# Kernel tuning notes

Hardware: AMD Instinct MI355X
Metric: run time of the kernel (lower is better)

Reference implementation:

```python
import jax, jax.numpy as jnp
import numpy as np

D_MODEL = 512
H = 8
D_K = D_MODEL // H


def setup_inputs() -> dict:
    key = jax.random.key(0)
    ks = jax.random.split(key, 11)
    B, S = 2, 2048
    scale = 1.0 / np.sqrt(D_MODEL)
    return {
        "q": jax.random.normal(ks[0], (B, S, D_MODEL), jnp.float32),
        "v": jax.random.normal(ks[1], (B, S, D_MODEL), jnp.float32),
        "k": jax.random.normal(ks[2], (B, S, D_MODEL), jnp.float32),
        "w_q": jax.random.normal(ks[3], (D_MODEL, D_MODEL), jnp.float32) * scale,
        "b_q": jnp.zeros((D_MODEL,), jnp.float32),
        "w_k": jax.random.normal(ks[4], (D_MODEL, D_MODEL), jnp.float32) * scale,
        "b_k": jnp.zeros((D_MODEL,), jnp.float32),
        "w_v": jax.random.normal(ks[5], (D_MODEL, D_MODEL), jnp.float32) * scale,
        "b_v": jnp.zeros((D_MODEL,), jnp.float32),
        "w_o": jax.random.normal(ks[6], (D_MODEL, D_MODEL), jnp.float32) * scale,
        "b_o": jnp.zeros((D_MODEL,), jnp.float32),
    }


def reference(q, v, k, w_q, b_q, w_k, b_k, w_v, b_v, w_o, b_o):
    B, S, _ = q.shape
    # projections (nn.Linear: x @ W.T + b)
    query = q @ w_q.T + b_q
    key_t = k @ w_k.T + b_k
    value = v @ w_v.T + b_v
    # split heads: [B, S, H, D_K] -> [B, H, S, D_K]
    query = query.reshape(B, S, H, D_K).transpose(0, 2, 1, 3)
    key_t = key_t.reshape(B, S, H, D_K).transpose(0, 2, 1, 3)
    value = value.reshape(B, S, H, D_K).transpose(0, 2, 1, 3)
    # unfused attention: full [B, H, S, S] score matrix
    scores = jnp.einsum("bhqd,bhkd->bhqk", query, key_t) / jnp.sqrt(
        jnp.asarray(D_K, query.dtype)
    )
    attn = jax.nn.softmax(scores, axis=-1)  # dropout inactive in eval
    x = jnp.einsum("bhqk,bhkd->bhqd", attn, value)
    # merge heads and output projection
    x = x.transpose(0, 2, 1, 3).reshape(B, S, D_MODEL)
    return x @ w_o.T + b_o
```

## Files before the change

kernel.cpp:

```cpp
#include <hip/hip_runtime.h>
#include <hip/hip_bf16.h>


typedef __attribute__((ext_vector_type(8))) short short8;
typedef __attribute__((ext_vector_type(4))) short short4v;
typedef __attribute__((ext_vector_type(4))) float f32x4;
typedef __attribute__((ext_vector_type(2))) unsigned int uint2v;

#define DM 512
#define SEQ 2048
#define NROW 4096
#define LOG2E 1.44269504088896341f
#define MFMA(a, b, c) __builtin_amdgcn_mfma_f32_16x16x32_bf16(a, b, c, 0, 0, 0)
#define FENCE() __asm__ __volatile__("" ::: "memory")

#if __has_builtin(__builtin_amdgcn_exp2f)
#define EXP2(x) __builtin_amdgcn_exp2f(x)
#else
#define EXP2(x) exp2f(x)
#endif

__device__ __forceinline__ float bf_bits2f(short s) {
    unsigned int u = ((unsigned int)(unsigned short)s) << 16;
    return __builtin_bit_cast(float, u);
}
__device__ __forceinline__ short f2bf_r(float f) {
    unsigned int u = __builtin_bit_cast(unsigned int, f) + 0x8000u;
    return (short)(u >> 16);
}
__device__ __forceinline__ unsigned int pack_bf16(float lo, float hi) {
    unsigned int ul = __builtin_bit_cast(unsigned int, lo) + 0x8000u;
    unsigned int uh = __builtin_bit_cast(unsigned int, hi) + 0x8000u;
    return __builtin_amdgcn_perm(uh, ul, 0x07060302u);
}

__device__ __forceinline__ void gload_lds16(const void* src, void* lds_dst) {
    __builtin_amdgcn_global_load_lds(
        (const __attribute__((address_space(1))) unsigned int*)src,
        (__attribute__((address_space(3))) unsigned int*)lds_dst, 16, 0, 0);
}

template <int ROWS, int NW>
__device__ __forceinline__ void stage_tile(const short* __restrict__ gsrc, size_t gstride,
                                           short* lds, int wave, int lane) {
    constexpr int ISSUES = ROWS * 8 / (64 * NW);
    #pragma unroll
    for (int i = 0; i < ISSUES; i++) {
        const int blk = i * NW + wave;
        const int g = blk * 64 + lane;
        const int row = g >> 3;
        const int cb = (g & 7) ^ (row & 7);
        gload_lds16(gsrc + (size_t)row * gstride + cb * 8, lds + (size_t)blk * 512);
    }
}

__device__ __forceinline__ bool detect_f32(const unsigned int* __restrict__ q, int* cnt_lds) {
    if (threadIdx.x == 0) *cnt_lds = 0;
    __syncthreads();
    int local = 0;
    for (int i = threadIdx.x; i < 1024; i += blockDim.x) {
        unsigned int lo = q[i] & 0x7FFFu;
        if (lo >= 0x3000u && lo < 0x4400u) local++;
    }
    if (local) atomicAdd(cnt_lds, local);
    __syncthreads();
    return *cnt_lds < 512;
}

struct ConvArgs { const void* src[11]; short* dst[11]; int n[11]; };
__global__ void convert_all(ConvArgs a) {
    __shared__ int cnt;
    const bool f32m = detect_f32((const unsigned int*)a.src[0], &cnt);
    const int tid = blockIdx.x * 256 + threadIdx.x;
    const int stride = gridDim.x * 256;
    if (f32m) {
        for (int s = 0; s < 11; s++) {
            const float4* sp = (const float4*)a.src[s];
            short4v* dp = (short4v*)a.dst[s];
            const int n4 = a.n[s] >> 2;
            for (int i = tid; i < n4; i += stride) {
                float4 v = sp[i];
                short4v o;
                o[0] = f2bf_r(v.x); o[1] = f2bf_r(v.y);
                o[2] = f2bf_r(v.z); o[3] = f2bf_r(v.w);
                dp[i] = o;
            }
        }
    } else {
        for (int s = 0; s < 11; s++) {
            const short4v* sp = (const short4v*)a.src[s];
            short4v* dp = (short4v*)a.dst[s];
            const int n4 = a.n[s] >> 2;
            for (int i = tid; i < n4; i += stride) dp[i] = sp[i];
        }
    }
}

template <int MT>
__device__ __forceinline__ void gemm_core(const short* __restrict__ A,
                                          const short* __restrict__ W,
                                          int m0, int n0, short* Alds, short* Blds,
                                          int wave, int lane, f32x4 (&acc)[MT / 64][4]) {
    const int rc = lane & 15, quad = lane >> 4;
    const short* Ag = A + (size_t)m0 * DM;
    const short* Bg = W + (size_t)n0 * DM;
    constexpr int ABUF = MT * 64, BBUF = 64 * 64;
    constexpr int INFLIGHT = MT * 8 / 256 + 2;
    constexpr int NITER = DM / 64;

    stage_tile<MT, 4>(Ag, DM, Alds, wave, lane);
    stage_tile<64, 4>(Bg, DM, Blds, wave, lane);

    for (int i = 0; i < NITER; i++) {
        const int cur = i & 1;
        const short* Ac = Alds + cur * ABUF;
        const short* Bc = Blds + cur * BBUF;
        if (i + 1 < NITER) {
            stage_tile<MT, 4>(Ag + (i + 1) * 64, DM, Alds + (cur ^ 1) * ABUF, wave, lane);
            stage_tile<64, 4>(Bg + (i + 1) * 64, DM, Blds + (cur ^ 1) * BBUF, wave, lane);
            __builtin_amdgcn_s_waitcnt(0x3F70 | INFLIGHT);
        } else {
            __builtin_amdgcn_s_waitcnt(0x3F70);
        }
        FENCE();
        __builtin_amdgcn_s_barrier();
        FENCE();
        #pragma unroll
        for (int h = 0; h < 2; h++) {
            short8 bf[4];
            #pragma unroll
            for (int nt = 0; nt < 4; nt++) {
                const int br = nt * 16 + rc;
                bf[nt] = *(const short8*)&Bc[br * 64 + (((quad + 4 * h) ^ (br & 7)) * 8)];
            }
            #pragma unroll
            for (int ms = 0; ms < MT / 64; ms++) {
                const int ar = wave * (MT / 4) + ms * 16 + rc;
                short8 af = *(const short8*)&Ac[ar * 64 + (((quad + 4 * h) ^ (ar & 7)) * 8)];
                #pragma unroll
                for (int nt = 0; nt < 4; nt++)
                    acc[ms][nt] = MFMA(af, bf[nt], acc[ms][nt]);
            }
        }
        FENCE();
        __builtin_amdgcn_s_barrier();
        FENCE();
    }
}

struct QKVArgs {
    const short* A[3]; const short* W[3]; const short* Bi[3];
    short* Cq; short* Ck; short* Cv;
};
__global__ __launch_bounds__(256, 3) void qkv_gemm(QKVArgs args) {
    __shared__ __align__(16) short Alds[2][128 * 64];
    __shared__ __align__(16) short Blds[2][64 * 64];
    const int z = blockIdx.z;
    const int wave = threadIdx.x >> 6, lane = threadIdx.x & 63;
    const int rc = lane & 15, quad = lane >> 4;
    const int m0 = blockIdx.x * 128, n0 = blockIdx.y * 64;

    f32x4 acc[2][4] = {};
    gemm_core<128>(args.A[z], args.W[z], m0, n0, &Alds[0][0], &Blds[0][0], wave, lane, acc);
    const short* bias = args.Bi[z];

    if (z == 2) {
        const int hh = n0 >> 6;
        #pragma unroll
        for (int ms = 0; ms < 2; ms++) {
            const int mw = m0 + wave * 32 + ms * 16;
            const int b = mw >> 11, sb = (mw & 2047) + quad * 4;
            #pragma unroll
            for (int nt = 0; nt < 4; nt++) {
                const int d = nt * 16 + rc;
                const float bv = bf_bits2f(bias[n0 + d]);
                short4v pk;
                #pragma unroll
                for (int r = 0; r < 4; r++) pk[r] = f2bf_r(acc[ms][nt][r] + bv);
                *(short4v*)(args.Cv + ((size_t)((b * 8 + hh) * 64 + d)) * SEQ + sb) = pk;
            }
        }
    } else {
        short* C = (z == 0) ? args.Cq : args.Ck;
        const float sc = (z == 0) ? (0.125f * LOG2E) : 1.0f;
        #pragma unroll
        for (int ms = 0; ms < 2; ms++) {
            const int mw = m0 + wave * 32 + ms * 16;
            #pragma unroll
            for (int nt = 0; nt < 4; nt++) {
                const int col = n0 + nt * 16 + rc;
                const float bv = bf_bits2f(bias[col]);
                #pragma unroll
                for (int r = 0; r < 4; r++)
                    C[(size_t)(mw + quad * 4 + r) * DM + col] = f2bf_r((acc[ms][nt][r] + bv) * sc);
            }
        }
    }
}

__global__ __launch_bounds__(256, 4) void out_gemm(
    const short* __restrict__ A, const short* __restrict__ W,
    const short* __restrict__ bias, void* __restrict__ Cout,
    const unsigned int* __restrict__ qraw) {
    __shared__ __align__(16) short Alds[2][64 * 64];
    __shared__ __align__(16) short Blds[2][64 * 64];
    __shared__ int cnt;
    const bool f32out = detect_f32(qraw, &cnt);
    const int wave = threadIdx.x >> 6, lane = threadIdx.x & 63;
    const int rc = lane & 15, quad = lane >> 4;
    const int m0 = blockIdx.x * 64, n0 = blockIdx.y * 64;
    f32x4 acc[1][4] = {};
    gemm_core<64>(A, W, m0, n0, &Alds[0][0], &Blds[0][0], wave, lane, acc);
    const int mw = m0 + wave * 16;
    #pragma unroll
    for (int nt = 0; nt < 4; nt++) {
        const int col = n0 + nt * 16 + rc;
        const float bv = bf_bits2f(bias[col]);
        #pragma unroll
        for (int r = 0; r < 4; r++) {
            const size_t idx = (size_t)(mw + quad * 4 + r) * DM + col;
            const float val = acc[0][nt][r] + bv;
            if (f32out) ((float*)Cout)[idx] = val;
            else        ((short*)Cout)[idx] = f2bf_r(val);
        }
    }
}

__global__ __launch_bounds__(256, 2) void attn_kernel(
    const short* __restrict__ Q, const short* __restrict__ K,
    const short* __restrict__ Vt, float* __restrict__ Opart,
    float* __restrict__ Lpart)
{
    __shared__ __align__(16) short Klds[2][64 * 64];
    __shared__ __align__(16) short Vlds[2][64 * 64];
    __shared__ __align__(16) short Plds[4][32 * 72];

    const int wave = threadIdx.x >> 6, lane = threadIdx.x & 63;
    const int rc = lane & 15, quad = lane >> 4;
    const int bh = blockIdx.y, z = blockIdx.z;
    const size_t baseQ = (size_t)(bh >> 3) * SEQ * DM + (size_t)(bh & 7) * 64;
    const short* Qb = Q + baseQ;
    const short* Kb = K + baseQ + (size_t)(z * 1024) * DM;
    const short* Vb = Vt + (size_t)bh * 64 * SEQ + z * 1024;
    const int q0 = blockIdx.x * 128 + wave * 32;

    short8 qa[2][2];
    #pragma unroll
    for (int ms = 0; ms < 2; ms++)
        #pragma unroll
        for (int h = 0; h < 2; h++)
            qa[ms][h] = *(const short8*)(Qb + (size_t)(q0 + ms * 16 + rc) * DM + h * 32 + quad * 8);

    short8 ones;
    #pragma unroll
    for (int j = 0; j < 8; j++) ones[j] = (short)0x3F80;

    f32x4 o[2][4] = {};
    f32x4 lsum[2] = {};
    short* Pw = &Plds[wave][0];

    int koff[4][2], voff[4][2];
    #pragma unroll
    for (int kt = 0; kt < 4; kt++) {
        const int row = rc * 4 + kt;
        #pragma unroll
        for (int h = 0; h < 2; h++)
            koff[kt][h] = row * 64 + (((quad + 4 * h) ^ (row & 7)) * 8);
    }
    #pragma unroll
    for (int dt = 0; dt < 4; dt++) {
        const int row = dt * 16 + rc;
        #pragma unroll
        for (int h = 0; h < 2; h++)
            voff[dt][h] = row * 64 + (((quad + 4 * h) ^ (row & 7)) * 8);
    }

    stage_tile<64, 4>(Kb, DM, &Klds[0][0], wave, lane);
    stage_tile<64, 4>(Vb, SEQ, &Vlds[0][0], wave, lane);

    auto body = [&](int it, int cur) {
        if (it + 1 < 16) {
            const int k0n = (it + 1) * 64;
            stage_tile<64, 4>(Kb + (size_t)k0n * DM, DM, &Klds[cur ^ 1][0], wave, lane);
            stage_tile<64, 4>(Vb + k0n, SEQ, &Vlds[cur ^ 1][0], wave, lane);
            __builtin_amdgcn_s_waitcnt(0x3F74);
        } else {
            __builtin_amdgcn_s_waitcnt(0x3F70);
        }
        FENCE();
        __builtin_amdgcn_s_barrier();
        FENCE();

        const short* Kt = &Klds[cur][0];
        const short* Vl = &Vlds[cur][0];

        short8 kf[4][2];
        #pragma unroll
        for (int kt = 0; kt < 4; kt++)
            #pragma unroll
            for (int h = 0; h < 2; h++)
                kf[kt][h] = *(const short8*)&Kt[koff[kt][h]];
        f32x4 s[2][4];
        #pragma unroll
        for (int ms = 0; ms < 2; ms++)
            #pragma unroll
            for (int kt = 0; kt < 4; kt++) {
                f32x4 t = {};
                t = MFMA(qa[ms][0], kf[kt][0], t);
                t = MFMA(qa[ms][1], kf[kt][1], t);
                s[ms][kt] = t;
            }
        #pragma unroll
        for (int ms = 0; ms < 2; ms++)
            #pragma unroll
            for (int r = 0; r < 4; r++) {
                uint2v pk;
                pk[0] = pack_bf16(EXP2(s[ms][0][r]), EXP2(s[ms][1][r]));
                pk[1] = pack_bf16(EXP2(s[ms][2][r]), EXP2(s[ms][3][r]));
                *(uint2v*)(&Pw[(ms * 16 + quad * 4 + r) * 72 + rc * 4]) = pk;
            }
        __builtin_amdgcn_s_waitcnt(0xC07F);
        short8 pa[2][2];
        #pragma unroll
        for (int ms = 0; ms < 2; ms++)
            #pragma unroll
            for (int h = 0; h < 2; h++)
                pa[ms][h] = *(const short8*)(&Pw[(ms * 16 + rc) * 72 + h * 32 + quad * 8]);
        #pragma unroll
        for (int ms = 0; ms < 2; ms++) {
            lsum[ms] = MFMA(pa[ms][0], ones, lsum[ms]);
            lsum[ms] = MFMA(pa[ms][1], ones, lsum[ms]);
        }
        #pragma unroll
        for (int dt = 0; dt < 4; dt++) {
            short8 v0 = *(const short8*)&Vl[voff[dt][0]];
            short8 v1 = *(const short8*)&Vl[voff[dt][1]];
            #pragma unroll
            for (int ms = 0; ms < 2; ms++) {
                o[ms][dt] = MFMA(pa[ms][0], v0, o[ms][dt]);
                o[ms][dt] = MFMA(pa[ms][1], v1, o[ms][dt]);
            }
        }
        FENCE();
        __builtin_amdgcn_s_barrier();
        FENCE();
    };

    for (int itp = 0; itp < 16; itp += 2) {
        body(itp, 0);
        body(itp + 1, 1);
    }

    const size_t obase = ((size_t)(z * 16 + bh)) * SEQ;
    #pragma unroll
    for (int ms = 0; ms < 2; ms++) {
        const int qrow = q0 + ms * 16 + quad * 4;
        if (rc == 0) {
            #pragma unroll
            for (int r = 0; r < 4; r++)
                Lpart[obase + qrow + r] = lsum[ms][r];
        }
        #pragma unroll
        for (int dt = 0; dt < 4; dt++)
            #pragma unroll
            for (int r = 0; r < 4; r++)
                Opart[(obase + qrow + r) * 64 + dt * 16 + rc] = o[ms][dt][r];
    }
}

__global__ void attn_reduce(const float* __restrict__ Opart, const float* __restrict__ Lpart,
                            short* __restrict__ X) {
    const int idx = blockIdx.x * 256 + threadIdx.x;
    const int dq = idx & 15;
    const int bhq = idx >> 4;
    const int bh = bhq >> 11, q = bhq & 2047;
    const float4 o0 = ((const float4*)Opart)[(size_t)bhq * 16 + dq];
    const float4 o1 = ((const float4*)Opart)[(size_t)(bhq + 16 * SEQ) * 16 + dq];
    const float inv = 1.0f / (Lpart[bhq] + Lpart[bhq + 16 * SEQ]);
    short4v pk;
    pk[0] = f2bf_r((o0.x + o1.x) * inv);
    pk[1] = f2bf_r((o0.y + o1.y) * inv);
    pk[2] = f2bf_r((o0.z + o1.z) * inv);
    pk[3] = f2bf_r((o0.w + o1.w) * inv);
    const size_t row = (size_t)(bh >> 3) * SEQ + q;
    *(short4v*)(&X[row * DM + (bh & 7) * 64 + dq * 4]) = pk;
}

extern "C" void kernel_launch(void* const* d_in, const int* in_sizes, int n_in,
                              void* d_out, int out_size, void* d_ws, size_t ws_size,
                              hipStream_t stream) {
    char* ws = (char*)d_ws;
    const size_t SEQB = (size_t)NROW * DM * sizeof(short);
    const size_t WB   = (size_t)DM * DM * sizeof(short);
    const size_t BB   = (size_t)DM * sizeof(short);

    size_t off = 0;
    short* qc = (short*)(ws + off); off += SEQB;
    short* vc = (short*)(ws + off); off += SEQB;
    short* kc = (short*)(ws + off); off += SEQB;
    short* wq = (short*)(ws + off); off += WB;
    short* wk = (short*)(ws + off); off += WB;
    short* wv = (short*)(ws + off); off += WB;
    short* wo = (short*)(ws + off); off += WB;
    short* bq = (short*)(ws + off); off += BB;
    short* bk = (short*)(ws + off); off += BB;
    short* bv = (short*)(ws + off); off += BB;
    short* bo = (short*)(ws + off); off += BB;
    off = (off + 255) & ~(size_t)255;
    short* Qp  = (short*)(ws + off); off += SEQB;
    short* Kp  = (short*)(ws + off); off += SEQB;
    short* Vtp = (short*)(ws + off); off += SEQB;
    short* Xp  = (short*)(ws + off); off += SEQB;
    float* Opart = (float*)(ws + off); off += (size_t)2 * 16 * SEQ * 64 * sizeof(float);
    float* Lpart = (float*)(ws + off); off += (size_t)2 * 16 * SEQ * sizeof(float);

    ConvArgs ca;
    const void* srcs[11] = {d_in[0], d_in[1], d_in[2], d_in[3], d_in[5], d_in[7],
                            d_in[9], d_in[4], d_in[6], d_in[8], d_in[10]};
    short* dsts[11] = {qc, vc, kc, wq, wk, wv, wo, bq, bk, bv, bo};
    int ns[11] = {NROW * DM, NROW * DM, NROW * DM, DM * DM, DM * DM, DM * DM,
                  DM * DM, DM, DM, DM, DM};
    for (int i = 0; i < 11; i++) { ca.src[i] = srcs[i]; ca.dst[i] = dsts[i]; ca.n[i] = ns[i]; }
    convert_all<<<1024, 256, 0, stream>>>(ca);

    QKVArgs qa;
    qa.A[0] = qc; qa.A[1] = kc; qa.A[2] = vc;
    qa.W[0] = wq; qa.W[1] = wk; qa.W[2] = wv;
    qa.Bi[0] = bq; qa.Bi[1] = bk; qa.Bi[2] = bv;
    qa.Cq = Qp; qa.Ck = Kp; qa.Cv = Vtp;
    qkv_gemm<<<dim3(NROW / 128, DM / 64, 3), 256, 0, stream>>>(qa);

    attn_kernel<<<dim3(SEQ / 128, 16, 2), 256, 0, stream>>>(Qp, Kp, Vtp, Opart, Lpart);
    attn_reduce<<<dim3(16 * SEQ * 16 / 256), 256, 0, stream>>>(Opart, Lpart, Xp);

    out_gemm<<<dim3(NROW / 64, DM / 64), 256, 0, stream>>>(
        Xp, wo, bo, d_out, (const unsigned int*)d_in[0]);
}
```

Before: 152.4 us.

## Triple-buffer attention K/V tiles, skip bf16 copy pass, shrink convert grid

The attention kernel moves from double to triple buffering of K/V tiles in LDS. It prefetches two tiles ahead and relaxes the waitcnt so more global loads stay in flight. When inputs are already bf16, the convert kernel now exits early and the GEMMs read the raw input buffers directly, which removes a copy pass. The convert grid drops from 1024 to 256 blocks. The extra LDS for the third buffer may reduce attention occupancy, and the fp32 path now does more loop iterations per thread.

```diff
diff --git a/kernel.cpp b/kernel.cpp
--- a/kernel.cpp
+++ b/kernel.cpp
@@ -71,27 +71,19 @@
 __global__ void convert_all(ConvArgs a) {
     __shared__ int cnt;
     const bool f32m = detect_f32((const unsigned int*)a.src[0], &cnt);
+    if (!f32m) return;
     const int tid = blockIdx.x * 256 + threadIdx.x;
     const int stride = gridDim.x * 256;
-    if (f32m) {
-        for (int s = 0; s < 11; s++) {
-            const float4* sp = (const float4*)a.src[s];
-            short4v* dp = (short4v*)a.dst[s];
-            const int n4 = a.n[s] >> 2;
-            for (int i = tid; i < n4; i += stride) {
-                float4 v = sp[i];
-                short4v o;
-                o[0] = f2bf_r(v.x); o[1] = f2bf_r(v.y);
-                o[2] = f2bf_r(v.z); o[3] = f2bf_r(v.w);
-                dp[i] = o;
-            }
-        }
-    } else {
-        for (int s = 0; s < 11; s++) {
-            const short4v* sp = (const short4v*)a.src[s];
-            short4v* dp = (short4v*)a.dst[s];
-            const int n4 = a.n[s] >> 2;
-            for (int i = tid; i < n4; i += stride) dp[i] = sp[i];
+    for (int s = 0; s < 11; s++) {
+        const float4* sp = (const float4*)a.src[s];
+        short4v* dp = (short4v*)a.dst[s];
+        const int n4 = a.n[s] >> 2;
+        for (int i = tid; i < n4; i += stride) {
+            float4 v = sp[i];
+            short4v o;
+            o[0] = f2bf_r(v.x); o[1] = f2bf_r(v.y);
+            o[2] = f2bf_r(v.z); o[3] = f2bf_r(v.w);
+            dp[i] = o;
         }
     }
 }
@@ -149,20 +141,26 @@
 }
 
 struct QKVArgs {
-    const short* A[3]; const short* W[3]; const short* Bi[3];
+    const short* Araw[3]; const short* Wraw[3]; const short* Braw[3];
+    const short* Acv[3];  const short* Wcv[3];  const short* Bcv[3];
     short* Cq; short* Ck; short* Cv;
+    const unsigned int* qraw;
 };
 __global__ __launch_bounds__(256, 3) void qkv_gemm(QKVArgs args) {
     __shared__ __align__(16) short Alds[2][128 * 64];
     __shared__ __align__(16) short Blds[2][64 * 64];
+    __shared__ int cnt;
+    const bool f32m = detect_f32(args.qraw, &cnt);
     const int z = blockIdx.z;
+    const short* A    = f32m ? args.Acv[z] : args.Araw[z];
+    const short* W    = f32m ? args.Wcv[z] : args.Wraw[z];
+    const short* bias = f32m ? args.Bcv[z] : args.Braw[z];
     const int wave = threadIdx.x >> 6, lane = threadIdx.x & 63;
     const int rc = lane & 15, quad = lane >> 4;
     const int m0 = blockIdx.x * 128, n0 = blockIdx.y * 64;
 
     f32x4 acc[2][4] = {};
-    gemm_core<128>(args.A[z], args.W[z], m0, n0, &Alds[0][0], &Blds[0][0], wave, lane, acc);
-    const short* bias = args.Bi[z];
+    gemm_core<128>(A, W, m0, n0, &Alds[0][0], &Blds[0][0], wave, lane, acc);
 
     if (z == 2) {
         const int hh = n0 >> 6;
@@ -199,13 +197,16 @@
 }
 
 __global__ __launch_bounds__(256, 4) void out_gemm(
-    const short* __restrict__ A, const short* __restrict__ W,
-    const short* __restrict__ bias, void* __restrict__ Cout,
+    const short* __restrict__ A, const short* __restrict__ Wraw,
+    const short* __restrict__ Wcv, const short* __restrict__ Braw,
+    const short* __restrict__ Bcv, void* __restrict__ Cout,
     const unsigned int* __restrict__ qraw) {
     __shared__ __align__(16) short Alds[2][64 * 64];
     __shared__ __align__(16) short Blds[2][64 * 64];
     __shared__ int cnt;
-    const bool f32out = detect_f32(qraw, &cnt);
+    const bool f32m = detect_f32(qraw, &cnt);
+    const short* W    = f32m ? Wcv : Wraw;
+    const short* bias = f32m ? Bcv : Braw;
     const int wave = threadIdx.x >> 6, lane = threadIdx.x & 63;
     const int rc = lane & 15, quad = lane >> 4;
     const int m0 = blockIdx.x * 64, n0 = blockIdx.y * 64;
@@ -220,8 +221,8 @@
         for (int r = 0; r < 4; r++) {
             const size_t idx = (size_t)(mw + quad * 4 + r) * DM + col;
             const float val = acc[0][nt][r] + bv;
-            if (f32out) ((float*)Cout)[idx] = val;
-            else        ((short*)Cout)[idx] = f2bf_r(val);
+            if (f32m) ((float*)Cout)[idx] = val;
+            else      ((short*)Cout)[idx] = f2bf_r(val);
         }
     }
 }
@@ -231,8 +232,8 @@
     const short* __restrict__ Vt, float* __restrict__ Opart,
     float* __restrict__ Lpart)
 {
-    __shared__ __align__(16) short Klds[2][64 * 64];
-    __shared__ __align__(16) short Vlds[2][64 * 64];
+    __shared__ __align__(16) short Klds[3][64 * 64];
+    __shared__ __align__(16) short Vlds[3][64 * 64];
     __shared__ __align__(16) short Plds[4][32 * 72];
 
     const int wave = threadIdx.x >> 6, lane = threadIdx.x & 63;
@@ -277,12 +278,17 @@
 
     stage_tile<64, 4>(Kb, DM, &Klds[0][0], wave, lane);
     stage_tile<64, 4>(Vb, SEQ, &Vlds[0][0], wave, lane);
+    stage_tile<64, 4>(Kb + (size_t)64 * DM, DM, &Klds[1][0], wave, lane);
+    stage_tile<64, 4>(Vb + 64, SEQ, &Vlds[1][0], wave, lane);
 
     auto body = [&](int it, int cur) {
-        if (it + 1 < 16) {
-            const int k0n = (it + 1) * 64;
-            stage_tile<64, 4>(Kb + (size_t)k0n * DM, DM, &Klds[cur ^ 1][0], wave, lane);
-            stage_tile<64, 4>(Vb + k0n, SEQ, &Vlds[cur ^ 1][0], wave, lane);
+        if (it < 14) {
+            const int k0n = (it + 2) * 64;
+            const int nb = (cur + 2) % 3;
+            stage_tile<64, 4>(Kb + (size_t)k0n * DM, DM, &Klds[nb][0], wave, lane);
+            stage_tile<64, 4>(Vb + k0n, SEQ, &Vlds[nb][0], wave, lane);
+            __builtin_amdgcn_s_waitcnt(0x3F78);
+        } else if (it == 14) {
             __builtin_amdgcn_s_waitcnt(0x3F74);
         } else {
             __builtin_amdgcn_s_waitcnt(0x3F70);
@@ -346,10 +352,12 @@
         FENCE();
     };
 
-    for (int itp = 0; itp < 16; itp += 2) {
+    for (int itp = 0; itp < 15; itp += 3) {
         body(itp, 0);
         body(itp + 1, 1);
-    }
+        body(itp + 2, 2);
+    }
+    body(15, 0);
 
     const size_t obase = ((size_t)(z * 16 + bh)) * SEQ;
     #pragma unroll
@@ -421,18 +429,23 @@
     int ns[11] = {NROW * DM, NROW * DM, NROW * DM, DM * DM, DM * DM, DM * DM,
                   DM * DM, DM, DM, DM, DM};
     for (int i = 0; i < 11; i++) { ca.src[i] = srcs[i]; ca.dst[i] = dsts[i]; ca.n[i] = ns[i]; }
-    convert_all<<<1024, 256, 0, stream>>>(ca);
+    convert_all<<<256, 256, 0, stream>>>(ca);
 
     QKVArgs qa;
-    qa.A[0] = qc; qa.A[1] = kc; qa.A[2] = vc;
-    qa.W[0] = wq; qa.W[1] = wk; qa.W[2] = wv;
-    qa.Bi[0] = bq; qa.Bi[1] = bk; qa.Bi[2] = bv;
+    qa.Araw[0] = (const short*)d_in[0]; qa.Araw[1] = (const short*)d_in[2]; qa.Araw[2] = (const short*)d_in[1];
+    qa.Wraw[0] = (const short*)d_in[3]; qa.Wraw[1] = (const short*)d_in[5]; qa.Wraw[2] = (const short*)d_in[7];
+    qa.Braw[0] = (const short*)d_in[4]; qa.Braw[1] = (const short*)d_in[6]; qa.Braw[2] = (const short*)d_in[8];
+    qa.Acv[0] = qc; qa.Acv[1] = kc; qa.Acv[2] = vc;
+    qa.Wcv[0] = wq; qa.Wcv[1] = wk; qa.Wcv[2] = wv;
+    qa.Bcv[0] = bq; qa.Bcv[1] = bk; qa.Bcv[2] = bv;
     qa.Cq = Qp; qa.Ck = Kp; qa.Cv = Vtp;
+    qa.qraw = (const unsigned int*)d_in[0];
     qkv_gemm<<<dim3(NROW / 128, DM / 64, 3), 256, 0, stream>>>(qa);
 
     attn_kernel<<<dim3(SEQ / 128, 16, 2), 256, 0, stream>>>(Qp, Kp, Vtp, Opart, Lpart);
     attn_reduce<<<dim3(16 * SEQ * 16 / 256), 256, 0, stream>>>(Opart, Lpart, Xp);
 
     out_gemm<<<dim3(NROW / 64, DM / 64), 256, 0, stream>>>(
-        Xp, wo, bo, d_out, (const unsigned int*)d_in[0]);
-}
+        Xp, (const short*)d_in[9], wo, (const short*)d_in[10], bo,
+        d_out, (const unsigned int*)d_in[0]);
+}
```

Result: slower. 157.1 us (+3.1%).
